# Kernel tuning notes

Hardware: AMD Instinct MI355X
Metric: run time of the kernel (lower is better)

Reference implementation:

```python
import jax, jax.numpy as jnp
import numpy as np

N_NODES = 100000
N_EDGES = 1600000
NUM_GRAPHS = 1024
IN_FEAT = 7
H = 128
NUM_LAYERS = 3
NUM_CLASSES = 2
BN_EPS = 1e-5


def _lin_init(key, fan_in, fan_out):
    kw, kb = jax.random.split(key)
    s = 1.0 / np.sqrt(fan_in)
    return (jax.random.normal(kw, (fan_in, fan_out), jnp.float32) * s,
            jax.random.normal(kb, (fan_out,), jnp.float32) * s)


def setup_inputs() -> dict:
    key = jax.random.key(0)
    ks = jax.random.split(key, 16)
    x = jax.random.normal(ks[0], (N_NODES, IN_FEAT), jnp.float32)
    edge_index = jax.random.randint(ks[1], (2, N_EDGES), 0, N_NODES, jnp.int32)
    batch = jnp.sort(jax.random.randint(ks[2], (N_NODES,), 0, NUM_GRAPHS, jnp.int32))

    inp = {"x": x, "edge_index": edge_index, "batch": batch}
    # GIN conv MLPs: layer 0 maps IN_FEAT->H->H, layers 1,2 map H->H->H
    fan = [IN_FEAT, H, H]
    for l in range(NUM_LAYERS):
        w1, b1 = _lin_init(ks[3 + 2 * l], fan[l], H)
        w2, b2 = _lin_init(ks[4 + 2 * l], H, H)
        inp[f"w1_{l}"], inp[f"b1_{l}"] = w1, b1
        inp[f"w2_{l}"], inp[f"b2_{l}"] = w2, b2
    # classifier MLP: [3*H, 2*H] + batchnorm(eval) + relu + [2*H, NUM_CLASSES]
    inp["clf_w1"], inp["clf_b1"] = _lin_init(ks[10], NUM_LAYERS * H, 2 * H)
    inp["clf_w2"], inp["clf_b2"] = _lin_init(ks[11], 2 * H, NUM_CLASSES)
    inp["bn_gamma"] = jnp.ones((2 * H,), jnp.float32)
    inp["bn_beta"] = jnp.zeros((2 * H,), jnp.float32)
    inp["bn_mean"] = jax.random.normal(ks[12], (2 * H,), jnp.float32) * 0.1
    inp["bn_var"] = jax.random.uniform(ks[13], (2 * H,), jnp.float32) + 0.5
    return inp


def _gin_conv(h, src, dst, w1, b1, w2, b2):
    # message = gather from source nodes, aggregate = scatter-sum onto target nodes
    agg = jax.ops.segment_sum(h[src], dst, num_segments=N_NODES)
    z = (1.0 + 0.0) * h + agg  # eps = 0 (train_eps=False)
    z = jax.nn.relu(z @ w1 + b1)  # dropout inside MLP is identity in eval
    return z @ w2 + b2


def reference(x, edge_index, batch,
              w1_0, b1_0, w2_0, b2_0,
              w1_1, b1_1, w2_1, b2_1,
              w1_2, b1_2, w2_2, b2_2,
              clf_w1, clf_b1, clf_w2, clf_b2,
              bn_gamma, bn_beta, bn_mean, bn_var):
    src, dst = edge_index[0], edge_index[1]
    params = [(w1_0, b1_0, w2_0, b2_0),
              (w1_1, b1_1, w2_1, b2_1),
              (w1_2, b1_2, w2_2, b2_2)]
    h = x
    xs = []
    for (w1, b1, w2, b2) in params:
        h = _gin_conv(h, src, dst, w1, b1, w2, b2)
        h = jax.nn.relu(h)  # BasicGNN post-conv act (dropout off in eval)
        xs.append(h)
    h = jnp.concatenate(xs, axis=-1)  # jk='cat' -> [N, 3H]
    g = jax.ops.segment_sum(h, batch, num_segments=NUM_GRAPHS)  # global_add_pool
    z = g @ clf_w1 + clf_b1
    z = (z - bn_mean) * jax.lax.rsqrt(bn_var + BN_EPS) * bn_gamma + bn_beta
    z = jax.nn.relu(z)
    return z @ clf_w2 + clf_b2  # [NUM_GRAPHS, NUM_CLASSES]
```

## Files before the change

kernel.cpp:

```cpp
#include <hip/hip_runtime.h>

#define N_NODESC    100000
#define N_EDGESC    1600000
#define NUM_GRAPHSC 1024
#define IN_FEATC    7
#define HDIM        128
#define N_TENSORS   21

#define NB       391
#define CHUNK_A  6250

typedef short s16x8 __attribute__((ext_vector_type(8)));
typedef float f32x4 __attribute__((ext_vector_type(4)));
typedef unsigned short u16x8 __attribute__((ext_vector_type(8)));

#if defined(__has_builtin)
# if __has_builtin(__builtin_amdgcn_cvt_pk_f32_fp8) && __has_builtin(__builtin_amdgcn_cvt_pk_fp8_f32)
#  define USE_HW_FP8 1
# endif
#endif

__global__ void GINModel_15058155340592_kernel() {
}

__device__ __forceinline__ float b2f(unsigned short u){
  union { unsigned int i; float f; } v;
  v.i = ((unsigned int)u) << 16;
  return v.f;
}
__device__ __forceinline__ unsigned short f2b(float f){
  union { float f; unsigned int i; } v;
  v.f = f;
  unsigned int x = v.i;
  return (unsigned short)((x + 0x7fffu + ((x >> 16) & 1u)) >> 16);
}

__device__ __forceinline__ unsigned char enc_fp8(float h){
  float x = fminf(h * 0.125f, 448.f);
#ifdef USE_HW_FP8
  int r = __builtin_amdgcn_cvt_pk_fp8_f32(x, x, 0, false);
  return (unsigned char)(r & 0xFF);
#else
  union { float f; unsigned int i; } u; u.f = x;
  unsigned b = u.i;
  b += 0x7FFFF + ((b >> 20) & 1);
  int e = (int)((b >> 23) & 0xFF) - 120;
  unsigned m = (b >> 20) & 7;
  if (e <= 0) return 0;
  if (e > 15) return 0x7E;
  return (unsigned char)((e << 3) | m);
#endif
}

__device__ __forceinline__ void acc_fp8x4(unsigned int u, float* a){
#ifdef USE_HW_FP8
  auto lo = __builtin_amdgcn_cvt_pk_f32_fp8((int)u, false);
  auto hi = __builtin_amdgcn_cvt_pk_f32_fp8((int)u, true);
  a[0] += lo[0]; a[1] += lo[1]; a[2] += hi[0]; a[3] += hi[1];
#else
  #pragma unroll
  for (int k = 0; k < 4; ++k){
    unsigned b = (u >> (k * 8)) & 0xFF;
    unsigned e = (b >> 3) & 0xF;
    unsigned m = b & 7;
    union { unsigned int i; float f; } w;
    w.i = ((e + 120) << 23) | (m << 20);
    float v = (e == 0) ? (float)m * 0.001953125f : w.f;
    a[k] += v;
  }
#endif
}

__global__ void k_detect(const unsigned short* xb, int* flag, int* bcnt){
  __shared__ int sh[256];
  int t = threadIdx.x;
  for (int i = t; i < 512; i += 256) bcnt[i] = 0;
  int cnt = 0;
  for (int i = t; i < 512; i += 256){
    unsigned e = (xb[i] >> 7) & 0xFF;
    if (e >= 0x68 && e <= 0x85) ++cnt;
  }
  sh[t] = cnt;
  __syncthreads();
  for (int s = 128; s > 0; s >>= 1){
    if (t < s) sh[t] += sh[t + s];
    __syncthreads();
  }
  if (t == 0) *flag = (sh[0] >= 400) ? 1 : 0;
}

struct CvtDesc { const void* src; int n; int off; };
struct CvtTable { CvtDesc d[N_TENSORS]; int total; };

__global__ void k_bhist(const int* dst, int* bcnt){
  __shared__ int h[NB];
  int tid = threadIdx.x;
  for (int i = tid; i < NB; i += 256) h[i] = 0;
  __syncthreads();
  int beg = blockIdx.x * CHUNK_A;
  int end = beg + CHUNK_A < N_EDGESC ? beg + CHUNK_A : N_EDGESC;
  for (int e = beg + tid; e < end; e += 256)
    atomicAdd(&h[dst[e] >> 8], 1);
  __syncthreads();
  for (int i = tid; i < NB; i += 256)
    if (h[i]) atomicAdd(&bcnt[i], h[i]);
}

__global__ void k_c2(const int* bcnt, int* bbase, int* bcursor, int* rowstart,
                     const int* batch, int* gs){
  if (blockIdx.x == 0){
    __shared__ int sh[512];
    int t = threadIdx.x;
    int v = (t < NB) ? bcnt[t] : 0;
    sh[t] = v;
    __syncthreads();
    for (int off = 1; off < 512; off <<= 1){
      int a = (t >= off) ? sh[t - off] : 0;
      __syncthreads();
      sh[t] += a;
      __syncthreads();
    }
    int excl = sh[t] - v;
    if (t < NB){ bbase[t] = excl; bcursor[t] = excl; }
    if (t == NB) bbase[NB] = sh[t];
    if (t == 0) rowstart[N_NODESC] = N_EDGESC;
  } else {
    int n = (blockIdx.x - 1) * 512 + threadIdx.x;
    if (n >= N_NODESC) return;
    int b = batch[n];
    if (n == 0){
      for (int g = 0; g <= b; ++g) gs[g] = 0;
    } else {
      int pb = batch[n - 1];
      if (pb != b){
        for (int g = pb + 1; g <= b; ++g) gs[g] = n;
      }
    }
    if (n == N_NODESC - 1){
      for (int g = b + 1; g <= NUM_GRAPHSC; ++g) gs[g] = N_NODESC;
    }
  }
}

__global__ void k_bscatter(const int* src, const int* dst, int* bcursor,
                           unsigned int* barr){
  __shared__ int lhist[NB];
  __shared__ int lbase[NB];
  int tid = threadIdx.x;
  for (int i = tid; i < NB; i += 256) lhist[i] = 0;
  __syncthreads();
  int beg = blockIdx.x * CHUNK_A;
  int end = beg + CHUNK_A < N_EDGESC ? beg + CHUNK_A : N_EDGESC;
  for (int e = beg + tid; e < end; e += 256)
    atomicAdd(&lhist[dst[e] >> 8], 1);
  __syncthreads();
  for (int b = tid; b < NB; b += 256){
    int c = lhist[b];
    lbase[b] = c ? atomicAdd(&bcursor[b], c) : 0;
  }
  __syncthreads();
  for (int i = tid; i < NB; i += 256) lhist[i] = 0;
  __syncthreads();
  for (int e = beg + tid; e < end; e += 256){
    int d = dst[e];
    int b = d >> 8;
    int ofs = atomicAdd(&lhist[b], 1);
    barr[lbase[b] + ofs] = ((unsigned)(d & 255) << 17) | (unsigned)src[e];
  }
}

__global__ void k_c4(const unsigned int* barr, const int* bbase,
                     int* rowstart, int* csr,
                     CvtTable T, unsigned short* pool, const int* flag){
  if (blockIdx.x < NB){
    __shared__ int h[256];
    __shared__ int sc[256];
    __shared__ int cur[256];
    int tid = threadIdx.x;
    int b = blockIdx.x;
    int beg = bbase[b];
    int end = bbase[b + 1];
    int n0 = b << 8;
    h[tid] = 0;
    __syncthreads();
    for (int i = beg + tid; i < end; i += 256)
      atomicAdd(&h[barr[i] >> 17], 1);
    __syncthreads();
    int v = h[tid];
    sc[tid] = v;
    __syncthreads();
    for (int off = 1; off < 256; off <<= 1){
      int a = (tid >= off) ? sc[tid - off] : 0;
      __syncthreads();
      sc[tid] += a;
      __syncthreads();
    }
    int excl = sc[tid] - v;
    int node = n0 + tid;
    if (node < N_NODESC) rowstart[node] = beg + excl;
    cur[tid] = beg + excl;
    __syncthreads();
    for (int i = beg + tid; i < end; i += 256){
      unsigned int e = barr[i];
      int local = e >> 17;
      int slot = atomicAdd(&cur[local], 1);
      csr[slot] = (int)(e & 0x1FFFF) << 7;
    }
  } else {
    int i = (blockIdx.x - NB) * 256 + threadIdx.x;
    if (i >= T.total) return;
    int isbf = *flag;
    for (int j = 0; j < N_TENSORS; ++j){
      int o = T.d[j].off;
      if (i >= o && i < o + T.d[j].n){
        int k = i - o;
        if (isbf) pool[i] = ((const unsigned short*)T.d[j].src)[k];
        else      pool[i] = f2b(((const float*)T.d[j].src)[k]);
        return;
      }
    }
  }
}

__global__ void k_l0(const unsigned short* x, const int* rs, const int* csr,
                     const unsigned short* w1, const unsigned short* b1,
                     unsigned short* t){
  __shared__ float sw[IN_FEATC * HDIM];
  __shared__ float sb[HDIM];
  int tid = threadIdx.x;
  for (int i = tid; i < IN_FEATC * HDIM; i += 256) sw[i] = b2f(w1[i]);
  if (tid < HDIM) sb[tid] = b2f(b1[tid]);
  __syncthreads();

  int n = blockIdx.x * 4 + (tid >> 6);
  int lane = tid & 63;
  int es = lane >> 3;
  int f  = lane & 7;
  int beg = rs[n];
  int end = rs[n + 1];
  bool fok = (f < IN_FEATC);
  float a = 0.f;
  for (int i = beg + es; i < end; i += 8){
    int s = csr[i] >> 7;
    if (fok) a += b2f(x[(size_t)s * IN_FEATC + f]);
  }
  if (es == 0 && fok) a += b2f(x[(size_t)n * IN_FEATC + f]);
  a += __shfl_xor(a, 8);
  a += __shfl_xor(a, 16);
  a += __shfl_xor(a, 32);
  float z[IN_FEATC];
  #pragma unroll
  for (int k = 0; k < IN_FEATC; ++k) z[k] = __shfl(a, k);
  int c0 = lane * 2;
  float acc0 = sb[c0];
  float acc1 = sb[c0 + 1];
  #pragma unroll
  for (int k = 0; k < IN_FEATC; ++k){
    acc0 += z[k] * sw[k * HDIM + c0];
    acc1 += z[k] * sw[k * HDIM + c0 + 1];
  }
  unsigned int pk = ((unsigned)f2b(fmaxf(acc1, 0.f)) << 16)
                  | (unsigned)f2b(fmaxf(acc0, 0.f));
  *(unsigned int*)(t + ((size_t)n << 7) + c0) = pk;
}

__global__ __launch_bounds__(256, 2)
void k_gemm128m(const unsigned short* A, const unsigned short* W,
                const unsigned short* bias, unsigned short* C, int ntiles)
{
  int wave = threadIdx.x >> 6;
  int lane = threadIdx.x & 63;
  int quad = lane >> 4;
  int l16  = lane & 15;

  union BU { s16x8 v; unsigned short s[8]; };
  BU bf[4][8];
  #pragma unroll
  for (int ks = 0; ks < 4; ++ks)
    #pragma unroll
    for (int ct = 0; ct < 8; ++ct){
      int c = ct * 16 + l16;
      #pragma unroll
      for (int j = 0; j < 8; ++j)
        bf[ks][ct].s[j] = W[(ks * 32 + quad * 8 + j) * HDIM + c];
    }

  float bv[8];
  #pragma unroll
  for (int ct = 0; ct < 8; ++ct) bv[ct] = b2f(bias[ct * 16 + l16]);

  for (int tile = blockIdx.x; tile < ntiles; tile += gridDim.x){
    int r = tile * 64 + wave * 16 + l16;
    BU af[4];
    if (r < N_NODESC){
      const unsigned short* arow = A + (size_t)r * HDIM;
      #pragma unroll
      for (int ks = 0; ks < 4; ++ks)
        af[ks].v = *reinterpret_cast<const s16x8*>(arow + ks * 32 + quad * 8);
    } else {
      #pragma unroll
      for (int ks = 0; ks < 4; ++ks)
        #pragma unroll
        for (int j = 0; j < 8; ++j) af[ks].s[j] = 0;
    }
    f32x4 acc[8];
    #pragma unroll
    for (int ct = 0; ct < 8; ++ct) acc[ct] = f32x4{0.f, 0.f, 0.f, 0.f};
    #pragma unroll
    for (int ks = 0; ks < 4; ++ks)
      #pragma unroll
      for (int ct = 0; ct < 8; ++ct)
        acc[ct] = __builtin_amdgcn_mfma_f32_16x16x32_bf16(af[ks].v, bf[ks][ct].v,
                                                          acc[ct], 0, 0, 0);

    int orow = tile * 64 + wave * 16 + quad * 4;
    #pragma unroll
    for (int ct = 0; ct < 8; ++ct){
      int c = ct * 16 + l16;
      #pragma unroll
      for (int rr = 0; rr < 4; ++rr){
        int row = orow + rr;
        if (row < N_NODESC)
          C[(size_t)row * HDIM + c] = f2b(fmaxf(acc[ct][rr] + bv[ct], 0.f));
      }
    }
  }
}

__global__ void k_agg128(const unsigned short* hin, const unsigned char* t8,
                         const int* rs, const int* csr, unsigned short* zout){
  int lane = threadIdx.x & 63;
  int slot = lane >> 4;
  int fl   = lane & 15;
  int n = blockIdx.x * 16 + (threadIdx.x >> 6) * 4 + slot;
  const unsigned char* hb8 = t8 + fl * 8;
  int beg = rs[n];
  int end = rs[n + 1];
  float a[8] = {0.f, 0.f, 0.f, 0.f, 0.f, 0.f, 0.f, 0.f};
  int i = beg;
  for (; i + 4 <= end; i += 4){
    int o0 = csr[i + 0];
    int o1 = csr[i + 1];
    int o2 = csr[i + 2];
    int o3 = csr[i + 3];
    uint2 v0 = *(const uint2*)(hb8 + o0);
    uint2 v1 = *(const uint2*)(hb8 + o1);
    uint2 v2 = *(const uint2*)(hb8 + o2);
    uint2 v3 = *(const uint2*)(hb8 + o3);
    acc_fp8x4(v0.x, a); acc_fp8x4(v0.y, a + 4);
    acc_fp8x4(v1.x, a); acc_fp8x4(v1.y, a + 4);
    acc_fp8x4(v2.x, a); acc_fp8x4(v2.y, a + 4);
    acc_fp8x4(v3.x, a); acc_fp8x4(v3.y, a + 4);
  }
  for (; i < end; ++i){
    int o = csr[i];
    uint2 v = *(const uint2*)(hb8 + o);
    acc_fp8x4(v.x, a); acc_fp8x4(v.y, a + 4);
  }
  u16x8 vs = *(const u16x8*)(hin + ((size_t)n << 7) + fl * 8);
  u16x8 o;
  #pragma unroll
  for (int j = 0; j < 8; ++j) o[j] = f2b(a[j] * 8.f + b2f(vs[j]));
  *(u16x8*)(zout + ((size_t)n << 7) + fl * 8) = o;
}

__global__ void k_pool_l(const unsigned short* __restrict__ h,
                         const int* __restrict__ gs,
                         float* __restrict__ pooled, int coloff,
                         unsigned char* __restrict__ c8){
  __shared__ float sh[256];
  int g = blockIdx.x;
  int t = threadIdx.x;
  int col = t & 127;
  int par = t >> 7;
  int s = gs[g];
  int e = gs[g + 1];
  const unsigned short* hp = h + col;
  float a0 = 0.f, a1 = 0.f, a2 = 0.f, a3 = 0.f;
  if (c8){
    unsigned char* cp = c8 + col;
    int n = s + par;
    for (; n + 6 < e; n += 8){
      float v0 = b2f(hp[(size_t)(n + 0) << 7]);
      float v1 = b2f(hp[(size_t)(n + 2) << 7]);
      float v2 = b2f(hp[(size_t)(n + 4) << 7]);
      float v3 = b2f(hp[(size_t)(n + 6) << 7]);
      cp[(size_t)(n + 0) << 7] = enc_fp8(v0);
      cp[(size_t)(n + 2) << 7] = enc_fp8(v1);
      cp[(size_t)(n + 4) << 7] = enc_fp8(v2);
      cp[(size_t)(n + 6) << 7] = enc_fp8(v3);
      a0 += v0; a1 += v1; a2 += v2; a3 += v3;
    }
    for (; n < e; n += 2){
      float v = b2f(hp[(size_t)n << 7]);
      cp[(size_t)n << 7] = enc_fp8(v);
      a0 += v;
    }
  } else {
    int n = s + par;
    for (; n + 6 < e; n += 8){
      a0 += b2f(hp[(size_t)(n + 0) << 7]);
      a1 += b2f(hp[(size_t)(n + 2) << 7]);
      a2 += b2f(hp[(size_t)(n + 4) << 7]);
      a3 += b2f(hp[(size_t)(n + 6) << 7]);
    }
    for (; n < e; n += 2) a0 += b2f(hp[(size_t)n << 7]);
  }
  sh[t] = (a0 + a1) + (a2 + a3);
  __syncthreads();
  if (t < 128)
    pooled[(size_t)g * 384 + coloff + t] = sh[t] + sh[t + 128];
}

__global__ void k_clf(const float* pooled,
                      const unsigned short* w1, const unsigned short* b1,
                      const unsigned short* w2, const unsigned short* b2c,
                      const unsigned short* gamma, const unsigned short* beta,
                      const unsigned short* mean, const unsigned short* var,
                      void* dout, const int* flag){
  __shared__ float sg[384];
  __shared__ float st[256];
  __shared__ float red[256];
  int g = blockIdx.x;
  int t = threadIdx.x;
  for (int i = t; i < 384; i += 256) sg[i] = pooled[(size_t)g * 384 + i];
  __syncthreads();
  const unsigned short* wp = w1 + t;
  float acc = b2f(b1[t]);
  #pragma unroll 4
  for (int k = 0; k < 384; ++k) acc += sg[k] * b2f(wp[k * 256]);
  float zb = (acc - b2f(mean[t])) * rsqrtf(b2f(var[t]) + 1e-5f) * b2f(gamma[t]) + b2f(beta[t]);
  st[t] = fmaxf(zb, 0.f);
  __syncthreads();
  for (int c = 0; c < 2; ++c){
    red[t] = st[t] * b2f(w2[t * 2 + c]);
    __syncthreads();
    for (int s = 128; s > 0; s >>= 1){
      if (t < s) red[t] += red[t + s];
      __syncthreads();
    }
    if (t == 0){
      float v = red[0] + b2f(b2c[c]);
      if (*flag) ((unsigned short*)dout)[g * 2 + c] = f2b(v);
      else       ((float*)dout)[g * 2 + c] = v;
    }
    __syncthreads();
  }
}

extern "C" void kernel_launch(void* const* d_in, const int* in_sizes, int n_in,
                              void* d_out, int out_size, void* d_ws, size_t ws_size,
                              hipStream_t stream)
{
  const int* ei    = (const int*)d_in[1];
  const int* batch = (const int*)d_in[2];
  (void)n_in; (void)out_size; (void)ws_size;

  char* w = (char*)d_ws;
  int* bcnt     = (int*)(w + 0);
  int* bbase    = (int*)(w + 2048);
  int* bcursor  = (int*)(w + 4096);
  int* rowstart = (int*)(w + 6144);
  int* gstart   = (int*)(w + 406272);
  int* flag     = (int*)(w + 410624);
  unsigned int* barr = (unsigned int*)(w + 410752);
  float* pooled = (float*)(w + 4010752);
  int* csr      = (int*)(w + 6810752);
  unsigned short* bufP = (unsigned short*)(w + 13210752);
  unsigned short* bufQ = (unsigned short*)(w + 38810752);
  unsigned short* pool = (unsigned short*)(w + 64410752);
  unsigned char* t8    = (unsigned char*)(w + 66410752);

  static const int order[N_TENSORS] =
      {0, 3, 4, 5, 6, 7, 8, 9, 10, 11, 12, 13, 14, 15, 16, 17, 18, 19, 20, 21, 22};
  CvtTable T;
  const unsigned short* pp[23];
  int off = 0;
  for (int j = 0; j < N_TENSORS; ++j){
    int i = order[j];
    T.d[j].src = d_in[i];
    T.d[j].n = in_sizes[i];
    T.d[j].off = off;
    pp[i] = pool + off;
    off += in_sizes[i];
  }
  T.total = off;

  const unsigned short* px = pp[0];
  const unsigned short* pw1[3] = {pp[3], pp[7],  pp[11]};
  const unsigned short* pb1[3] = {pp[4], pp[8],  pp[12]};
  const unsigned short* pw2[3] = {pp[5], pp[9],  pp[13]};
  const unsigned short* pb2[3] = {pp[6], pp[10], pp[14]};

  const int* src = ei;
  const int* dst = ei + N_EDGESC;
  int ntiles = (N_NODESC + 63) / 64;
  int ncvt = (T.total + 255) / 256;
  int nc2 = 1 + (N_NODESC + 511) / 512;

  k_detect<<<dim3(1), dim3(256), 0, stream>>>((const unsigned short*)d_in[0], flag, bcnt);

  k_bhist<<<dim3(256), dim3(256), 0, stream>>>(dst, bcnt);
  k_c2<<<dim3(nc2), dim3(512), 0, stream>>>(bcnt, bbase, bcursor, rowstart, batch, gstart);
  k_bscatter<<<dim3(256), dim3(256), 0, stream>>>(src, dst, bcursor, barr);
  k_c4<<<dim3(NB + ncvt), dim3(256), 0, stream>>>(barr, bbase, rowstart, csr, T, pool, flag);

  k_l0<<<dim3(N_NODESC / 4), dim3(256), 0, stream>>>(px, rowstart, csr, pw1[0], pb1[0], bufP);
  k_gemm128m<<<dim3(782), dim3(256), 0, stream>>>(bufP, pw2[0], pb2[0], bufP, ntiles);
  k_pool_l<<<dim3(NUM_GRAPHSC), dim3(256), 0, stream>>>(bufP, gstart, pooled, 0, t8);

  k_agg128<<<dim3(N_NODESC / 16), dim3(256), 0, stream>>>(bufP, t8, rowstart, csr, bufQ);
  k_gemm128m<<<dim3(782), dim3(256), 0, stream>>>(bufQ, pw1[1], pb1[1], bufQ, ntiles);
  k_gemm128m<<<dim3(782), dim3(256), 0, stream>>>(bufQ, pw2[1], pb2[1], bufQ, ntiles);
  k_pool_l<<<dim3(NUM_GRAPHSC), dim3(256), 0, stream>>>(bufQ, gstart, pooled, 128, t8);

  k_agg128<<<dim3(N_NODESC / 16), dim3(256), 0, stream>>>(bufQ, t8, rowstart, csr, bufP);
  k_gemm128m<<<dim3(782), dim3(256), 0, stream>>>(bufP, pw1[2], pb1[2], bufP, ntiles);
  k_gemm128m<<<dim3(782), dim3(256), 0, stream>>>(bufP, pw2[2], pb2[2], bufP, ntiles);
  k_pool_l<<<dim3(NUM_GRAPHSC), dim3(256), 0, stream>>>(bufP, gstart, pooled, 256, (unsigned char*)nullptr);

  k_clf<<<dim3(NUM_GRAPHSC), dim3(256), 0, stream>>>(pooled, pp[15], pp[16], pp[17], pp[18],
                                                     pp[19], pp[20], pp[21], pp[22],
                                                     d_out, flag);
}
```

Baseline: 430.6 us.

## Pad layer-0 features to 8 bf16 and restructure gather with two threads per node

```diff
diff --git a/kernel.cpp b/kernel.cpp
--- a/kernel.cpp
+++ b/kernel.cpp
@@ -5,7 +5,7 @@
 #define NUM_GRAPHSC 1024
 #define IN_FEATC    7
 #define HDIM        128
-#define N_TENSORS   21
+#define N_TENSORS   20
 
 #define NB       391
 #define CHUNK_A  6250
@@ -71,6 +71,15 @@
 #endif
 }
 
+__device__ __forceinline__ void acc_bf4(uint2 v, float& a0, float& a1,
+                                        float& a2, float& a3){
+  union { unsigned int i; float f; } t;
+  t.i = v.x << 16;          a0 += t.f;
+  t.i = v.x & 0xffff0000u;  a1 += t.f;
+  t.i = v.y << 16;          a2 += t.f;
+  t.i = v.y & 0xffff0000u;  a3 += t.f;
+}
+
 __global__ void k_detect(const unsigned short* xb, int* flag, int* bcnt){
   __shared__ int sh[256];
   int t = threadIdx.x;
@@ -222,46 +231,98 @@
   }
 }
 
-__global__ void k_l0(const unsigned short* x, const int* rs, const int* csr,
-                     const unsigned short* w1, const unsigned short* b1,
-                     unsigned short* t){
-  __shared__ float sw[IN_FEATC * HDIM];
-  __shared__ float sb[HDIM];
-  int tid = threadIdx.x;
-  for (int i = tid; i < IN_FEATC * HDIM; i += 256) sw[i] = b2f(w1[i]);
-  if (tid < HDIM) sb[tid] = b2f(b1[tid]);
-  __syncthreads();
-
-  int n = blockIdx.x * 4 + (tid >> 6);
+__global__ void k_padx(const void* xin, const int* flag, unsigned short* x8){
+  int n = blockIdx.x * 256 + threadIdx.x;
+  if (n >= N_NODESC) return;
+  u16x8 o;
+  if (*flag){
+    const unsigned short* s = (const unsigned short*)xin + (size_t)n * IN_FEATC;
+    #pragma unroll
+    for (int j = 0; j < IN_FEATC; ++j) o[j] = s[j];
+  } else {
+    const float* s = (const float*)xin + (size_t)n * IN_FEATC;
+    #pragma unroll
+    for (int j = 0; j < IN_FEATC; ++j) o[j] = f2b(s[j]);
+  }
+  o[7] = 0;
+  *(u16x8*)(x8 + (size_t)n * 8) = o;
+}
+
+__global__ __launch_bounds__(256)
+void k_l0(const unsigned short* x8, const int* rs, const int* csr,
+          const unsigned short* w1, const unsigned short* b1,
+          unsigned short* t){
+  __shared__ __align__(16) float sz[128 * 8];
+  int tid  = threadIdx.x;
   int lane = tid & 63;
-  int es = lane >> 3;
-  int f  = lane & 7;
-  int beg = rs[n];
-  int end = rs[n + 1];
-  bool fok = (f < IN_FEATC);
-  float a = 0.f;
-  for (int i = beg + es; i < end; i += 8){
-    int s = csr[i] >> 7;
-    if (fok) a += b2f(x[(size_t)s * IN_FEATC + f]);
-  }
-  if (es == 0 && fok) a += b2f(x[(size_t)n * IN_FEATC + f]);
-  a += __shfl_xor(a, 8);
-  a += __shfl_xor(a, 16);
-  a += __shfl_xor(a, 32);
-  float z[IN_FEATC];
-  #pragma unroll
-  for (int k = 0; k < IN_FEATC; ++k) z[k] = __shfl(a, k);
+  int wave = tid >> 6;
+  int p    = tid & 1;
+  int bn   = tid >> 1;
+  int n    = blockIdx.x * 128 + bn;
+
   int c0 = lane * 2;
-  float acc0 = sb[c0];
-  float acc1 = sb[c0 + 1];
+  float wa[IN_FEATC], wb[IN_FEATC];
   #pragma unroll
   for (int k = 0; k < IN_FEATC; ++k){
-    acc0 += z[k] * sw[k * HDIM + c0];
-    acc1 += z[k] * sw[k * HDIM + c0 + 1];
-  }
-  unsigned int pk = ((unsigned)f2b(fmaxf(acc1, 0.f)) << 16)
-                  | (unsigned)f2b(fmaxf(acc0, 0.f));
-  *(unsigned int*)(t + ((size_t)n << 7) + c0) = pk;
+    unsigned int u = *(const unsigned int*)(w1 + k * HDIM + c0);
+    union { unsigned int i; float f; } lo, hi;
+    lo.i = u << 16; hi.i = u & 0xffff0000u;
+    wa[k] = lo.f; wb[k] = hi.f;
+  }
+  unsigned int ub = *(const unsigned int*)(b1 + c0);
+  union { unsigned int i; float f; } blo, bhi;
+  blo.i = ub << 16; bhi.i = ub & 0xffff0000u;
+  float bv0 = blo.f, bv1 = bhi.f;
+
+  float a0 = 0.f, a1 = 0.f, a2 = 0.f, a3 = 0.f;
+  int beg = 0, end = 0;
+  if (n < N_NODESC){ beg = rs[n]; end = rs[n + 1]; }
+  const unsigned char* xb = (const unsigned char*)x8 + p * 8;
+  int i = beg;
+  for (; i + 4 <= end; i += 4){
+    int o0 = csr[i + 0];
+    int o1 = csr[i + 1];
+    int o2 = csr[i + 2];
+    int o3 = csr[i + 3];
+    uint2 v0 = *(const uint2*)(xb + (o0 >> 3));
+    uint2 v1 = *(const uint2*)(xb + (o1 >> 3));
+    uint2 v2 = *(const uint2*)(xb + (o2 >> 3));
+    uint2 v3 = *(const uint2*)(xb + (o3 >> 3));
+    acc_bf4(v0, a0, a1, a2, a3);
+    acc_bf4(v1, a0, a1, a2, a3);
+    acc_bf4(v2, a0, a1, a2, a3);
+    acc_bf4(v3, a0, a1, a2, a3);
+  }
+  for (; i < end; ++i){
+    uint2 v = *(const uint2*)(xb + (csr[i] >> 3));
+    acc_bf4(v, a0, a1, a2, a3);
+  }
+  if (n < N_NODESC){
+    uint2 v = *(const uint2*)((const unsigned char*)x8 + (size_t)n * 16 + p * 8);
+    acc_bf4(v, a0, a1, a2, a3);
+  }
+  *(f32x4*)&sz[bn * 8 + p * 4] = f32x4{a0, a1, a2, a3};
+  __syncthreads();
+
+  int j0 = wave * 32;
+  for (int j = 0; j < 32; ++j){
+    int no = blockIdx.x * 128 + j0 + j;
+    f32x4 z0 = *(const f32x4*)&sz[(j0 + j) * 8];
+    f32x4 z1 = *(const f32x4*)&sz[(j0 + j) * 8 + 4];
+    float acc0 = bv0, acc1 = bv1;
+    acc0 += z0[0] * wa[0]; acc1 += z0[0] * wb[0];
+    acc0 += z0[1] * wa[1]; acc1 += z0[1] * wb[1];
+    acc0 += z0[2] * wa[2]; acc1 += z0[2] * wb[2];
+    acc0 += z0[3] * wa[3]; acc1 += z0[3] * wb[3];
+    acc0 += z1[0] * wa[4]; acc1 += z1[0] * wb[4];
+    acc0 += z1[1] * wa[5]; acc1 += z1[1] * wb[5];
+    acc0 += z1[2] * wa[6]; acc1 += z1[2] * wb[6];
+    if (no < N_NODESC){
+      unsigned int pk = ((unsigned)f2b(fmaxf(acc1, 0.f)) << 16)
+                      | (unsigned)f2b(fmaxf(acc0, 0.f));
+      *(unsigned int*)(t + ((size_t)no << 7) + c0) = pk;
+    }
+  }
 }
 
 __global__ __launch_bounds__(256, 2)
@@ -464,6 +525,7 @@
   int* gstart   = (int*)(w + 406272);
   int* flag     = (int*)(w + 410624);
   unsigned int* barr = (unsigned int*)(w + 410752);
+  unsigned short* x8 = (unsigned short*)(w + 410752);
   float* pooled = (float*)(w + 4010752);
   int* csr      = (int*)(w + 6810752);
   unsigned short* bufP = (unsigned short*)(w + 13210752);
@@ -472,7 +534,7 @@
   unsigned char* t8    = (unsigned char*)(w + 66410752);
 
   static const int order[N_TENSORS] =
-      {0, 3, 4, 5, 6, 7, 8, 9, 10, 11, 12, 13, 14, 15, 16, 17, 18, 19, 20, 21, 22};
+      {3, 4, 5, 6, 7, 8, 9, 10, 11, 12, 13, 14, 15, 16, 17, 18, 19, 20, 21, 22};
   CvtTable T;
   const unsigned short* pp[23];
   int off = 0;
@@ -486,7 +548,6 @@
   }
   T.total = off;
 
-  const unsigned short* px = pp[0];
   const unsigned short* pw1[3] = {pp[3], pp[7],  pp[11]};
   const unsigned short* pb1[3] = {pp[4], pp[8],  pp[12]};
   const unsigned short* pw2[3] = {pp[5], pp[9],  pp[13]};
@@ -505,7 +566,9 @@
   k_bscatter<<<dim3(256), dim3(256), 0, stream>>>(src, dst, bcursor, barr);
   k_c4<<<dim3(NB + ncvt), dim3(256), 0, stream>>>(barr, bbase, rowstart, csr, T, pool, flag);
 
-  k_l0<<<dim3(N_NODESC / 4), dim3(256), 0, stream>>>(px, rowstart, csr, pw1[0], pb1[0], bufP);
+  k_padx<<<dim3((N_NODESC + 255) / 256), dim3(256), 0, stream>>>(d_in[0], flag, x8);
+
+  k_l0<<<dim3((N_NODESC + 127) / 128), dim3(256), 0, stream>>>(x8, rowstart, csr, pw1[0], pb1[0], bufP);
   k_gemm128m<<<dim3(782), dim3(256), 0, stream>>>(bufP, pw2[0], pb2[0], bufP, ntiles);
   k_pool_l<<<dim3(NUM_GRAPHSC), dim3(256), 0, stream>>>(bufP, gstart, pooled, 0, t8);
 
```

After: 412.2 us. 1.04x faster.
